# Kernel optimization log

Measured on AMD Instinct MI355X. Metric: run time of the kernel, lower is better.

## Reference

```python
import jax, jax.numpy as jnp
import numpy as np
from jax import lax

B, C_IN, IMG, P, HID = 128, 3, 224, 16, 768
HW = (IMG // P) ** 2  # 196 patches


def setup_inputs() -> dict:
    key = jax.random.key(0)
    k1, k2, k3, k4 = jax.random.split(key, 4)
    x = jax.random.normal(k1, (B, C_IN, IMG, IMG), dtype=jnp.float32)
    # conv weight init scale ~ kaiming-ish, value irrelevant for correctness
    W = jax.random.normal(k2, (HID, C_IN, P, P), dtype=jnp.float32) * 0.02
    b = jax.random.normal(k3, (HID,), dtype=jnp.float32) * 0.02
    # per-sample random permutation of patch positions (the pixel shuffle)
    perm = jax.vmap(lambda k: jax.random.permutation(k, HW))(jax.random.split(k4, B)).astype(jnp.int32)
    return {"x": x, "W": W, "b": b, "perm": perm}


def reference(x, W, b, perm):
    # patchify conv: kernel_size == stride == P, no padding
    enc = lax.conv_general_dilated(
        x, W, window_strides=(P, P), padding="VALID",
        dimension_numbers=("NCHW", "OIHW", "NCHW"),
    ) + b[None, :, None, None]                      # [B, HID, H', W']
    Bc, Cc, Hc, Wc = enc.shape
    enc = enc.reshape(Bc, Cc, Hc * Wc).transpose(0, 2, 1)   # [B, HW, HID]
    # per-sample patch shuffle: shuffled[i, j] = enc[i, perm[i, j]]
    shuffled = jnp.take_along_axis(enc, perm[:, :, None], axis=1)
    return shuffled
```

## Files before the change

kernel.cpp:

```cpp
#include <hip/hip_runtime.h>
#include <hip/hip_bf16.h>

#define BATCH  128
#define HWN    196
#define HIDN   768
#define KN     768
#define IMGSZ  224
#define IMG2   (224*224)
#define MTOT   (BATCH*HWN)

#define BM 128
#define BN 128
#define BK 32
#define NT  (KN/BK)
#define NBM (MTOT/BM)
#define NBN (HIDN/BN)
#define NWG (NBM*NBN)
#define CPX (NWG/8)

typedef __attribute__((ext_vector_type(8))) short bf16x8;
typedef __attribute__((ext_vector_type(4))) float floatx4;

#define GP(p) ((const __attribute__((address_space(1))) void*)(p))
#define SP(p) ((__attribute__((address_space(3))) void*)(p))

static __device__ __forceinline__ short f2bf(float f) {
    __hip_bfloat16 h = __float2bfloat16(f);
    return __builtin_bit_cast(short, h);
}

static __device__ __forceinline__ bf16x8 cvt8v(float4 f0, float4 f1) {
    bf16x8 v;
    v[0]=f2bf(f0.x); v[1]=f2bf(f0.y); v[2]=f2bf(f0.z); v[3]=f2bf(f0.w);
    v[4]=f2bf(f1.x); v[5]=f2bf(f1.y); v[6]=f2bf(f1.z); v[7]=f2bf(f1.w);
    return v;
}

__global__ __launch_bounds__(256)
void prep_W(const float* __restrict__ W, unsigned short* __restrict__ Wb)
{
    const int idx = blockIdx.x * 256 + threadIdx.x;
    float4 f0 = *(const float4*)(W + (size_t)idx * 8);
    float4 f1 = *(const float4*)(W + (size_t)idx * 8 + 4);
    *(bf16x8*)(Wb + (size_t)idx * 8) = cvt8v(f0, f1);
}

__global__ __launch_bounds__(256, 3)
void gemm_fused(const float* __restrict__ x, const int* __restrict__ perm,
                const unsigned short* __restrict__ Wb,
                const float* __restrict__ bias, float* __restrict__ out)
{
    __shared__ __align__(16) unsigned short As[BM * BK];
    __shared__ __align__(16) unsigned short Bs[BN * BK];

    const int tid = threadIdx.x;
    const int wg  = blockIdx.x;
    const int lid = (wg & 7) * CPX + (wg >> 3);
    const int bm  = lid / NBN;
    const int bn  = lid - bm * NBN;

    const int arow = tid >> 1;
    const int aseg = tid & 1;
    const int gr   = bm * BM + arow;
    const int b    = gr / HWN;
    const int p    = perm[gr];
    const int py   = p / 14, px = p - py * 14;
    const float* xbase = x + (size_t)b * 3 * IMG2
                           + (size_t)(py * 16) * IMGSZ + px * 16;
    const int axor = ((arow >> 1) & 1) << 4;
    char* aw0 = (char*)As + arow * 64 + ((aseg * 32     ) ^ axor);
    char* aw1 = (char*)As + arow * 64 + ((aseg * 32 + 16) ^ axor);

    const int srow = tid >> 2;
    const int sseg = tid & 3;
    const unsigned short* gb = Wb + (size_t)(bn * BN + srow) * KN + sseg * 8;

    const int lane = tid & 63;
    const int wave = tid >> 6;
    const int wm = (wave >> 1) * 64;
    const int wn = (wave & 1) * 64;
    const int lr = lane & 15;
    const int lq = lane >> 4;
    const int ard = (lq * 16) ^ (((lr >> 1) & 1) << 4);

    floatx4 acc[4][4] = {};
    float4 xf0, xf1, xf2, xf3;

    auto loadx = [&](int t) {
        const int s = t * 2 + aseg;
        const float* src = xbase + (s >> 4) * IMG2 + (s & 15) * IMGSZ;
        xf0 = *(const float4*)(src);
        xf1 = *(const float4*)(src + 4);
        xf2 = *(const float4*)(src + 8);
        xf3 = *(const float4*)(src + 12);
    };
    auto writea = [&]() {
        *(bf16x8*)aw0 = cvt8v(xf0, xf1);
        *(bf16x8*)aw1 = cvt8v(xf2, xf3);
    };
    auto gldsb = [&](int t) {
        __builtin_amdgcn_global_load_lds(GP(gb + t * BK),           SP(&Bs[tid * 8]),        16, 0, 0);
        __builtin_amdgcn_global_load_lds(GP(gb + 64 * KN + t * BK), SP(&Bs[2048 + tid * 8]), 16, 0, 0);
    };

    loadx(0);
    gldsb(0);
    writea();
    __syncthreads();

    for (int t = 0; t < NT; ++t) {
        if (t + 1 < NT) loadx(t + 1);

        bf16x8 bfrag[4];
        #pragma unroll
        for (int j = 0; j < 4; ++j)
            bfrag[j] = *(const bf16x8*)&Bs[(wn + j * 16 + lr) * BK + lq * 8];
        #pragma unroll
        for (int i = 0; i < 4; ++i) {
            const bf16x8 afrag = *(const bf16x8*)((const char*)As + (wm + i * 16 + lr) * 64 + ard);
            #pragma unroll
            for (int j = 0; j < 4; ++j)
                acc[i][j] = __builtin_amdgcn_mfma_f32_16x16x32_bf16(
                                afrag, bfrag[j], acc[i][j], 0, 0, 0);
        }

        if (t + 1 < NT) {
            __syncthreads();
            gldsb(t + 1);
            writea();
            __syncthreads();
        }
    }

    #pragma unroll
    for (int j = 0; j < 4; ++j) {
        const int gc = bn * BN + wn + j * 16 + lr;
        const float bv = bias[gc];
        #pragma unroll
        for (int i = 0; i < 4; ++i) {
            const int grow = bm * BM + wm + i * 16 + lq * 4;
            float* op = out + (size_t)grow * HIDN + gc;
            #pragma unroll
            for (int r = 0; r < 4; ++r)
                op[(size_t)r * HIDN] = acc[i][j][r] + bv;
        }
    }
}

extern "C" void kernel_launch(void* const* d_in, const int* in_sizes, int n_in,
                              void* d_out, int out_size, void* d_ws, size_t ws_size,
                              hipStream_t stream) {
    const float* x    = (const float*)d_in[0];
    const float* W    = (const float*)d_in[1];
    const float* bias = (const float*)d_in[2];
    const int*   perm = (const int*)d_in[3];
    float* out = (float*)d_out;

    unsigned short* Wb = (unsigned short*)d_ws;

    prep_W<<<dim3(KN * HIDN / 8 / 256), dim3(256), 0, stream>>>(W, Wb);
    gemm_fused<<<dim3(NWG), dim3(256), 0, stream>>>(x, perm, Wb, bias, out);
}
```

Measured before the change: 212.1 us.

## Double-buffer A tile in LDS, load W fragments directly to registers, prefetch x two steps ahead

Replaces the single-buffered A/B LDS tiles with a double-buffered A tile so each K step needs one barrier instead of two. The B (weight) fragments are now read straight from global memory into registers one step ahead instead of being staged through LDS via global_load_lds. The x loads are software-pipelined two iterations deep. This aims to cut barrier stalls and LDS traffic, at the cost of more registers (which may hurt occupancy under launch_bounds 256,3) and redundant global W reads across waves that share the same columns.

```diff
diff --git a/kernel.cpp b/kernel.cpp
--- a/kernel.cpp
+++ b/kernel.cpp
@@ -21,9 +21,6 @@
 typedef __attribute__((ext_vector_type(8))) short bf16x8;
 typedef __attribute__((ext_vector_type(4))) float floatx4;
 
-#define GP(p) ((const __attribute__((address_space(1))) void*)(p))
-#define SP(p) ((__attribute__((address_space(3))) void*)(p))
-
 static __device__ __forceinline__ short f2bf(float f) {
     __hip_bfloat16 h = __float2bfloat16(f);
     return __builtin_bit_cast(short, h);
@@ -35,6 +32,8 @@
     v[4]=f2bf(f1.x); v[5]=f2bf(f1.y); v[6]=f2bf(f1.z); v[7]=f2bf(f1.w);
     return v;
 }
+
+struct xs16 { float4 a, b, c, d; };
 
 __global__ __launch_bounds__(256)
 void prep_W(const float* __restrict__ W, unsigned short* __restrict__ Wb)
@@ -50,8 +49,7 @@
                 const unsigned short* __restrict__ Wb,
                 const float* __restrict__ bias, float* __restrict__ out)
 {
-    __shared__ __align__(16) unsigned short As[BM * BK];
-    __shared__ __align__(16) unsigned short Bs[BN * BK];
+    __shared__ __align__(16) unsigned short As[2][BM * BK];
 
     const int tid = threadIdx.x;
     const int wg  = blockIdx.x;
@@ -67,13 +65,9 @@
     const int py   = p / 14, px = p - py * 14;
     const float* xbase = x + (size_t)b * 3 * IMG2
                            + (size_t)(py * 16) * IMGSZ + px * 16;
-    const int axor = ((arow >> 1) & 1) << 4;
-    char* aw0 = (char*)As + arow * 64 + ((aseg * 32     ) ^ axor);
-    char* aw1 = (char*)As + arow * 64 + ((aseg * 32 + 16) ^ axor);
-
-    const int srow = tid >> 2;
-    const int sseg = tid & 3;
-    const unsigned short* gb = Wb + (size_t)(bn * BN + srow) * KN + sseg * 8;
+    const int axor  = ((arow >> 1) & 1) << 4;
+    const int aoff0 = arow * 64 + ((aseg * 32     ) ^ axor);
+    const int aoff1 = arow * 64 + ((aseg * 32 + 16) ^ axor);
 
     const int lane = tid & 63;
     const int wave = tid >> 6;
@@ -83,54 +77,74 @@
     const int lq = lane >> 4;
     const int ard = (lq * 16) ^ (((lr >> 1) & 1) << 4);
 
+    const unsigned short* wrow0 = Wb + (size_t)(bn * BN + wn +  0 + lr) * KN + lq * 8;
+    const unsigned short* wrow1 = Wb + (size_t)(bn * BN + wn + 16 + lr) * KN + lq * 8;
+    const unsigned short* wrow2 = Wb + (size_t)(bn * BN + wn + 32 + lr) * KN + lq * 8;
+    const unsigned short* wrow3 = Wb + (size_t)(bn * BN + wn + 48 + lr) * KN + lq * 8;
+
     floatx4 acc[4][4] = {};
-    float4 xf0, xf1, xf2, xf3;
 
-    auto loadx = [&](int t) {
+    auto loadx = [&](int t) -> xs16 {
         const int s = t * 2 + aseg;
         const float* src = xbase + (s >> 4) * IMG2 + (s & 15) * IMGSZ;
-        xf0 = *(const float4*)(src);
-        xf1 = *(const float4*)(src + 4);
-        xf2 = *(const float4*)(src + 8);
-        xf3 = *(const float4*)(src + 12);
+        xs16 r;
+        r.a = *(const float4*)(src);
+        r.b = *(const float4*)(src + 4);
+        r.c = *(const float4*)(src + 8);
+        r.d = *(const float4*)(src + 12);
+        return r;
     };
-    auto writea = [&]() {
-        *(bf16x8*)aw0 = cvt8v(xf0, xf1);
-        *(bf16x8*)aw1 = cvt8v(xf2, xf3);
-    };
-    auto gldsb = [&](int t) {
-        __builtin_amdgcn_global_load_lds(GP(gb + t * BK),           SP(&Bs[tid * 8]),        16, 0, 0);
-        __builtin_amdgcn_global_load_lds(GP(gb + 64 * KN + t * BK), SP(&Bs[2048 + tid * 8]), 16, 0, 0);
+    auto writea = [&](unsigned short* buf, const xs16& v) {
+        *(bf16x8*)((char*)buf + aoff0) = cvt8v(v.a, v.b);
+        *(bf16x8*)((char*)buf + aoff1) = cvt8v(v.c, v.d);
     };
 
-    loadx(0);
-    gldsb(0);
-    writea();
+    bf16x8 bfr0, bfr1, bfr2, bfr3;
+    xs16 xq, xl;
+
+    xq = loadx(0);
+    bfr0 = *(const bf16x8*)(wrow0);
+    bfr1 = *(const bf16x8*)(wrow1);
+    bfr2 = *(const bf16x8*)(wrow2);
+    bfr3 = *(const bf16x8*)(wrow3);
+    writea(As[0], xq);
+    xq = loadx(1);
+    xl = loadx(2);
     __syncthreads();
 
-    for (int t = 0; t < NT; ++t) {
-        if (t + 1 < NT) loadx(t + 1);
+#define STEP(T, CUR, NXT)                                                     \
+    do {                                                                      \
+        const int t_ = (T);                                                   \
+        if (t_ + 1 < NT) writea(As[NXT], xq);                                 \
+        xq = xl;                                                              \
+        if (t_ + 3 < NT) xl = loadx(t_ + 3);                                  \
+        bf16x8 bnx0, bnx1, bnx2, bnx3;                                        \
+        if (t_ + 1 < NT) {                                                    \
+            bnx0 = *(const bf16x8*)(wrow0 + (t_ + 1) * BK);                   \
+            bnx1 = *(const bf16x8*)(wrow1 + (t_ + 1) * BK);                   \
+            bnx2 = *(const bf16x8*)(wrow2 + (t_ + 1) * BK);                   \
+            bnx3 = *(const bf16x8*)(wrow3 + (t_ + 1) * BK);                   \
+        }                                                                     \
+        _Pragma("unroll")                                                     \
+        for (int i = 0; i < 4; ++i) {                                         \
+            const bf16x8 afrag = *(const bf16x8*)((const char*)As[CUR]        \
+                                      + (wm + i * 16 + lr) * 64 + ard);       \
+            acc[i][0] = __builtin_amdgcn_mfma_f32_16x16x32_bf16(afrag, bfr0, acc[i][0], 0, 0, 0); \
+            acc[i][1] = __builtin_amdgcn_mfma_f32_16x16x32_bf16(afrag, bfr1, acc[i][1], 0, 0, 0); \
+            acc[i][2] = __builtin_amdgcn_mfma_f32_16x16x32_bf16(afrag, bfr2, acc[i][2], 0, 0, 0); \
+            acc[i][3] = __builtin_amdgcn_mfma_f32_16x16x32_bf16(afrag, bfr3, acc[i][3], 0, 0, 0); \
+        }                                                                     \
+        if (t_ + 1 < NT) {                                                    \
+            bfr0 = bnx0; bfr1 = bnx1; bfr2 = bnx2; bfr3 = bnx3;               \
+            __syncthreads();         \
+        }                                                                     \
+    } while (0)
 
-        bf16x8 bfrag[4];
-        #pragma unroll
-        for (int j = 0; j < 4; ++j)
-            bfrag[j] = *(const bf16x8*)&Bs[(wn + j * 16 + lr) * BK + lq * 8];
-        #pragma unroll
-        for (int i = 0; i < 4; ++i) {
-            const bf16x8 afrag = *(const bf16x8*)((const char*)As + (wm + i * 16 + lr) * 64 + ard);
-            #pragma unroll
-            for (int j = 0; j < 4; ++j)
-                acc[i][j] = __builtin_amdgcn_mfma_f32_16x16x32_bf16(
-                                afrag, bfrag[j], acc[i][j], 0, 0, 0);
-        }
-
-        if (t + 1 < NT) {
-            __syncthreads();
-            gldsb(t + 1);
-            writea();
-            __syncthreads();
-        }
+    for (int tt = 0; tt < NT; tt += 2) {
+        STEP(tt,     0, 1);
+        STEP(tt + 1, 1, 0);
     }
+#undef STEP
 
     #pragma unroll
     for (int j = 0; j < 4; ++j) {
```

Result: slower. 231.8 us (+9.3%).

## Stream fp32 image patches straight to LDS and convert to bf16 at fragment load

Applied to the files above, without the earlier changes.

The A operand (shuffled image patches) is now copied straight from global memory into LDS as fp32 using global_load_lds, with an XOR swizzle on the column index. The bf16 conversion moves into the fragment read path, so the register staging and the separate LDS write of converted values go away. In exchange, A tiles double in LDS size, each A fragment is converted repeatedly per wave, and the loop loses its prefetch of the next tile: loads are issued and then waited on each iteration, with no overlap between loading and MFMA.

```diff
diff --git a/kernel.cpp b/kernel.cpp
--- a/kernel.cpp
+++ b/kernel.cpp
@@ -50,7 +50,7 @@
                 const unsigned short* __restrict__ Wb,
                 const float* __restrict__ bias, float* __restrict__ out)
 {
-    __shared__ __align__(16) unsigned short As[BM * BK];
+    __shared__ __align__(16) float          As[BM * BK];
     __shared__ __align__(16) unsigned short Bs[BN * BK];
 
     const int tid = threadIdx.x;
@@ -59,17 +59,21 @@
     const int bm  = lid / NBN;
     const int bn  = lid - bm * NBN;
 
-    const int arow = tid >> 1;
-    const int aseg = tid & 1;
-    const int gr   = bm * BM + arow;
-    const int b    = gr / HWN;
-    const int p    = perm[gr];
-    const int py   = p / 14, px = p - py * 14;
-    const float* xbase = x + (size_t)b * 3 * IMG2
-                           + (size_t)(py * 16) * IMGSZ + px * 16;
-    const int axor = ((arow >> 1) & 1) << 4;
-    char* aw0 = (char*)As + arow * 64 + ((aseg * 32     ) ^ axor);
-    char* aw1 = (char*)As + arow * 64 + ((aseg * 32 + 16) ^ axor);
+    const int kl = (tid & 7) ^ ((tid >> 3) & 7);
+    const int s2 = kl >> 2;
+    const int k4 = kl & 3;
+    const float* pA0; const float* pA1; const float* pA2; const float* pA3;
+#define MKPA(PTR, G)                                                          \
+    do {                                                                      \
+        const int gr = bm * BM + (G) * 32 + (tid >> 3);                       \
+        const int b  = gr / HWN;                                              \
+        const int p  = perm[gr];                                              \
+        const int py = p / 14, px = p - py * 14;                              \
+        PTR = x + (size_t)b * 3 * IMG2 + (size_t)(py * 16 + s2) * IMGSZ       \
+                + px * 16 + k4 * 4;                                           \
+    } while (0)
+    MKPA(pA0, 0); MKPA(pA1, 1); MKPA(pA2, 2); MKPA(pA3, 3);
+#undef MKPA
 
     const int srow = tid >> 2;
     const int sseg = tid & 3;
@@ -81,35 +85,20 @@
     const int wn = (wave & 1) * 64;
     const int lr = lane & 15;
     const int lq = lane >> 4;
-    const int ard = (lq * 16) ^ (((lr >> 1) & 1) << 4);
+    const int aoffA = (((lq << 1)    ) ^ (lr & 7)) << 4;
+    const int aoffB = (((lq << 1) | 1) ^ (lr & 7)) << 4;
 
     floatx4 acc[4][4] = {};
-    float4 xf0, xf1, xf2, xf3;
 
-    auto loadx = [&](int t) {
-        const int s = t * 2 + aseg;
-        const float* src = xbase + (s >> 4) * IMG2 + (s & 15) * IMGSZ;
-        xf0 = *(const float4*)(src);
-        xf1 = *(const float4*)(src + 4);
-        xf2 = *(const float4*)(src + 8);
-        xf3 = *(const float4*)(src + 12);
-    };
-    auto writea = [&]() {
-        *(bf16x8*)aw0 = cvt8v(xf0, xf1);
-        *(bf16x8*)aw1 = cvt8v(xf2, xf3);
-    };
-    auto gldsb = [&](int t) {
-        __builtin_amdgcn_global_load_lds(GP(gb + t * BK),           SP(&Bs[tid * 8]),        16, 0, 0);
-        __builtin_amdgcn_global_load_lds(GP(gb + 64 * KN + t * BK), SP(&Bs[2048 + tid * 8]), 16, 0, 0);
-    };
-
-    loadx(0);
-    gldsb(0);
-    writea();
-    __syncthreads();
-
-    for (int t = 0; t < NT; ++t) {
-        if (t + 1 < NT) loadx(t + 1);
+    for (int it = 0; it < NT; ++it) {
+        const int off = (it >> 3) * IMG2 + (it & 7) * 448;
+        __builtin_amdgcn_global_load_lds(GP(pA0 + off), SP((char*)As +         tid * 16), 16, 0, 0);
+        __builtin_amdgcn_global_load_lds(GP(pA1 + off), SP((char*)As +  4096 + tid * 16), 16, 0, 0);
+        __builtin_amdgcn_global_load_lds(GP(pA2 + off), SP((char*)As +  8192 + tid * 16), 16, 0, 0);
+        __builtin_amdgcn_global_load_lds(GP(pA3 + off), SP((char*)As + 12288 + tid * 16), 16, 0, 0);
+        __builtin_amdgcn_global_load_lds(GP(gb + it * BK),           SP(&Bs[tid * 8]),        16, 0, 0);
+        __builtin_amdgcn_global_load_lds(GP(gb + 64 * KN + it * BK), SP(&Bs[2048 + tid * 8]), 16, 0, 0);
+        __syncthreads();
 
         bf16x8 bfrag[4];
         #pragma unroll
@@ -117,19 +106,16 @@
             bfrag[j] = *(const bf16x8*)&Bs[(wn + j * 16 + lr) * BK + lq * 8];
         #pragma unroll
         for (int i = 0; i < 4; ++i) {
-            const bf16x8 afrag = *(const bf16x8*)((const char*)As + (wm + i * 16 + lr) * 64 + ard);
+            const char* rbase = (const char*)As + (wm + i * 16 + lr) * 128;
+            float4 fa = *(const float4*)(rbase + aoffA);
+            float4 fb = *(const float4*)(rbase + aoffB);
+            const bf16x8 afrag = cvt8v(fa, fb);
             #pragma unroll
             for (int j = 0; j < 4; ++j)
                 acc[i][j] = __builtin_amdgcn_mfma_f32_16x16x32_bf16(
                                 afrag, bfrag[j], acc[i][j], 0, 0, 0);
         }
-
-        if (t + 1 < NT) {
-            __syncthreads();
-            gldsb(t + 1);
-            writea();
-            __syncthreads();
-        }
+        __syncthreads();
     }
 
     #pragma unroll
```

Result: faster. 196.0 us (-7.6%).
